# Kernel tuning notes

Measured on AMD Instinct MI355X. Metric: run time of the kernel, lower is better.

Reference implementation:

```python
import jax, jax.numpy as jnp
import numpy as np
import math

N = 12288
D = 64
SCALE0 = math.log(10.0)


def lorentz_linear(x, W, b, scale):
    # x: [N, D] -> nn.Linear then Lorentz re-normalization onto the hyperboloid
    h = x @ W.T + b
    time = jax.nn.sigmoid(h[:, :1]) * jnp.exp(scale) + 1.1  # [N, 1]
    xn = h[:, 1:]  # spatial components [N, D-1]
    sq = jnp.clip(jnp.sum(xn * xn, axis=-1, keepdims=True), 1e-8, None)
    s = (time * time - 1.0) / sq
    return jnp.concatenate([time, xn * jnp.sqrt(s)], axis=-1)


def setup_inputs() -> dict:
    key = jax.random.key(0)
    ks = jax.random.split(key, 8)
    stdv = 1.0 / math.sqrt(D)
    x = jax.random.normal(ks[0], (N, D), dtype=jnp.float32)
    # sparse-ish binary adjacency stored dense (module calls adj.to_dense())
    adj = (jax.random.uniform(ks[1], (N, N)) < 0.002).astype(jnp.float32)
    W = jax.random.uniform(ks[2], (D, D), minval=-stdv, maxval=stdv, dtype=jnp.float32)
    Wq = jax.random.uniform(ks[3], (D, D), minval=-stdv, maxval=stdv, dtype=jnp.float32)
    Wk = jax.random.uniform(ks[4], (D, D), minval=-stdv, maxval=stdv, dtype=jnp.float32)
    z = jnp.zeros((D,), dtype=jnp.float32)
    sc = jnp.asarray(SCALE0, dtype=jnp.float32)
    return {
        'x': x, 'adj': adj,
        'W': W, 'b': z, 'scale': sc,
        'Wq': Wq, 'bq': z, 'scale_q': sc,
        'Wk': Wk, 'bk': z, 'scale_k': sc,
        'att_bias': jnp.asarray(20.0, dtype=jnp.float32),
        'att_scale': jnp.asarray(math.sqrt(D), dtype=jnp.float32),
    }


def reference(x, adj, W, b, scale, Wq, bq, scale_q, Wk, bk, scale_k, att_bias, att_scale):
    # LorentzLinear
    h = lorentz_linear(x, W, b, scale)  # [N, D]
    # LorentzAgg with attention
    q = lorentz_linear(h, Wq, bq, scale_q)
    k = lorentz_linear(h, Wk, bk, scale_k)
    # cinner: Lorentzian inner product matrix (negate time component of q)
    qm = jnp.concatenate([-q[:, :1], q[:, 1:]], axis=-1)
    att = 2.0 + 2.0 * (qm @ k.T)                 # [N, N]
    att = jax.nn.sigmoid(att / att_scale + att_bias)
    att = adj * att                               # mask by adjacency
    support = att @ h                             # [N, D]
    # Lorentz self-inner: inner(v,v) = -v0^2 + sum(v_rest^2); denorm = sqrt(|-inner|)
    inner = -support[:, :1] ** 2 + jnp.sum(support[:, 1:] ** 2, axis=-1, keepdims=True)
    denorm = jnp.sqrt(jnp.clip(jnp.abs(-inner), 1e-8, None))
    return support / denorm
```

## Files before the change

### kernel.cpp

```cpp
#include <hip/hip_runtime.h>
#include <math.h>

#define N   12288
#define D   64
#define CAP 96
#define ITS ((N / 4) / 256)

typedef unsigned int uint4n __attribute__((ext_vector_type(4)));

__device__ __forceinline__ float wave_sum(float v) {
    #pragma unroll
    for (int m = 32; m >= 1; m >>= 1) v += __shfl_xor(v, m, 64);
    return v;
}
__device__ __forceinline__ float sigmoidf(float a) { return 1.0f / (1.0f + __expf(-a)); }

__global__ __launch_bounds__(256) void linear_kernel(
        const float* __restrict__ x,
        const float* __restrict__ W,  const float* __restrict__ b,  const float* __restrict__ scale,
        const float* __restrict__ Wq, const float* __restrict__ bq, const float* __restrict__ scale_q,
        const float* __restrict__ Wk, const float* __restrict__ bk, const float* __restrict__ scale_k,
        float* __restrict__ h, float* __restrict__ qm, float* __restrict__ kmat) {
    __shared__ float Wl [D * (D + 1)];
    __shared__ float Wql[D * (D + 1)];
    __shared__ float Wkl[D * (D + 1)];

    const int tid  = threadIdx.x;
    const int lane = tid & 63;
    const int w    = tid >> 6;
    const int row  = blockIdx.x * 4 + w;

    for (int idx = tid; idx < D * D; idx += 256) {
        int d = idx >> 6, kk = idx & 63;
        Wl [d * (D + 1) + kk] = W [idx];
        Wql[d * (D + 1) + kk] = Wq[idx];
        Wkl[d * (D + 1) + kk] = Wk[idx];
    }
    __syncthreads();

    float hvv;
    {
        float xv  = x[row * D + lane];
        float acc = b[lane];
        const float* wr = &Wl[lane * (D + 1)];
        #pragma unroll
        for (int kk = 0; kk < D; ++kk)
            acc = fmaf(__shfl(xv, kk, 64), wr[kk], acc);
        float h0   = __shfl(acc, 0, 64);
        float time = __expf(scale[0]) * sigmoidf(h0) + 1.1f;
        float sq   = fmaxf(wave_sum((lane == 0) ? 0.0f : acc * acc), 1e-8f);
        float r    = sqrtf((time * time - 1.0f) / sq);
        hvv = (lane == 0) ? time : acc * r;
        h[row * D + lane] = hvv;
    }

    {
        float accq = bq[lane], acck = bk[lane];
        const float* wq = &Wql[lane * (D + 1)];
        const float* wk = &Wkl[lane * (D + 1)];
        #pragma unroll
        for (int kk = 0; kk < D; ++kk) {
            float xk = __shfl(hvv, kk, 64);
            accq = fmaf(xk, wq[kk], accq);
            acck = fmaf(xk, wk[kk], acck);
        }
        {
            float h0   = __shfl(accq, 0, 64);
            float time = __expf(scale_q[0]) * sigmoidf(h0) + 1.1f;
            float sq   = fmaxf(wave_sum((lane == 0) ? 0.0f : accq * accq), 1e-8f);
            float r    = sqrtf((time * time - 1.0f) / sq);
            qm[row * D + lane] = (lane == 0) ? -time : accq * r;
        }
        {
            float h0   = __shfl(acck, 0, 64);
            float time = __expf(scale_k[0]) * sigmoidf(h0) + 1.1f;
            float sq   = fmaxf(wave_sum((lane == 0) ? 0.0f : acck * acck), 1e-8f);
            float r    = sqrtf((time * time - 1.0f) / sq);
            kmat[row * D + lane] = (lane == 0) ? time : acck * r;
        }
    }
}

__global__ __launch_bounds__(256) void adj_gather_kernel(
        const uint4n* __restrict__ adj4,
        const float* __restrict__ qm,
        const float* __restrict__ kmat,
        const float* __restrict__ h,
        const float* __restrict__ att_bias_p,
        const float* __restrict__ att_scale_p,
        float* __restrict__ out) {
    __shared__ int scols[CAP];
    __shared__ int scnt;
    __shared__ float sacc[4][D];

    int tid  = threadIdx.x;
    int row  = blockIdx.x;
    int lane = tid & 63;
    int w    = tid >> 6;
    if (tid == 0) scnt = 0;

    const uint4n* rowp = adj4 + (size_t)row * (N / 4);
    uint4n vv[ITS];
    #pragma unroll
    for (int it = 0; it < ITS; ++it)
        vv[it] = __builtin_nontemporal_load(&rowp[it * 256 + tid]);

    float qv        = qm[row * D + lane];
    float bias      = att_bias_p[0];
    float inv_scale = 1.0f / att_scale_p[0];
    __syncthreads();

    #pragma unroll
    for (int it = 0; it < ITS; ++it) {
        uint4n v = vv[it];
        if ((v.x | v.y | v.z | v.w) != 0u) {
            int t = it * 256 + tid;
            unsigned e[4] = {v.x, v.y, v.z, v.w};
            #pragma unroll
            for (int c = 0; c < 4; ++c) {
                if (e[c] != 0u) {
                    int pos = atomicAdd(&scnt, 1);
                    if (pos < CAP) scols[pos] = t * 4 + c;
                }
            }
        }
    }
    __syncthreads();

    int m = scnt; if (m > CAP) m = CAP;

    float acc = 0.0f;
    for (int n = w; n < m; n += 4) {
        int j = scols[n];
        float dot = wave_sum(qv * kmat[j * D + lane]);
        float att = sigmoidf(fmaf(2.0f + 2.0f * dot, inv_scale, bias));
        acc = fmaf(att, h[j * D + lane], acc);
    }
    sacc[w][lane] = acc;
    __syncthreads();

    if (w == 0) {
        float total = sacc[0][lane] + sacc[1][lane] + sacc[2][lane] + sacc[3][lane];
        float contrib = (lane == 0) ? -total * total : total * total;
        float inner   = wave_sum(contrib);
        float denorm  = sqrtf(fmaxf(fabsf(inner), 1e-8f));
        out[row * D + lane] = total / denorm;
    }
}

extern "C" void kernel_launch(void* const* d_in, const int* in_sizes, int n_in,
                              void* d_out, int out_size, void* d_ws, size_t ws_size,
                              hipStream_t stream) {
    const float*  x         = (const float*)d_in[0];
    const uint4n* adj       = (const uint4n*)d_in[1];
    const float*  W         = (const float*)d_in[2];
    const float*  b         = (const float*)d_in[3];
    const float*  scale     = (const float*)d_in[4];
    const float*  Wq        = (const float*)d_in[5];
    const float*  bq        = (const float*)d_in[6];
    const float*  scale_q   = (const float*)d_in[7];
    const float*  Wk        = (const float*)d_in[8];
    const float*  bk        = (const float*)d_in[9];
    const float*  scale_k   = (const float*)d_in[10];
    const float*  att_bias  = (const float*)d_in[11];
    const float*  att_scale = (const float*)d_in[12];
    float* out = (float*)d_out;

    float* h    = (float*)d_ws;
    float* qm   = h  + (size_t)N * D;
    float* kmat = qm + (size_t)N * D;

    linear_kernel<<<N / 4, 256, 0, stream>>>(x, W, b, scale,
                                             Wq, bq, scale_q, Wk, bk, scale_k,
                                             h, qm, kmat);
    adj_gather_kernel<<<N, 256, 0, stream>>>(adj, qm, kmat, h,
                                             att_bias, att_scale, out);
}
```

Baseline: 784.3 us.

## Split adjacency scan into grid-stride streaming kernel and separate gather kernel

Splits the fused per-row kernel into two. A grid-stride scan kernel streams the dense adjacency with deep unrolled nontemporal loads and appends nonzero column indices to per-row lists through global atomics. A separate gather kernel then reads those lists to compute attention and aggregate. The goal is to decouple the bandwidth-bound scan from per-row gather latency and keep more memory traffic in flight, and the gather loop also prefetches the next column index. The cost is an extra launch, global atomics and workspace for counts and columns.

```diff
diff --git a/kernel.cpp b/kernel.cpp
--- a/kernel.cpp
+++ b/kernel.cpp
@@ -4,7 +4,12 @@
 #define N   12288
 #define D   64
 #define CAP 96
-#define ITS ((N / 4) / 256)
+
+#define CHUNKS      (N * (N / 4))
+#define SCAN_BLOCKS 2048
+#define SCAN_UNROLL 8
+#define SCAN_STRIDE (SCAN_BLOCKS * 256)
+#define SCAN_PASSES (CHUNKS / (SCAN_STRIDE * SCAN_UNROLL))
 
 typedef unsigned int uint4n __attribute__((ext_vector_type(4)));
 
@@ -20,7 +25,8 @@
         const float* __restrict__ W,  const float* __restrict__ b,  const float* __restrict__ scale,
         const float* __restrict__ Wq, const float* __restrict__ bq, const float* __restrict__ scale_q,
         const float* __restrict__ Wk, const float* __restrict__ bk, const float* __restrict__ scale_k,
-        float* __restrict__ h, float* __restrict__ qm, float* __restrict__ kmat) {
+        float* __restrict__ h, float* __restrict__ qm, float* __restrict__ kmat,
+        int* __restrict__ cnt) {
     __shared__ float Wl [D * (D + 1)];
     __shared__ float Wql[D * (D + 1)];
     __shared__ float Wkl[D * (D + 1)];
@@ -29,6 +35,8 @@
     const int lane = tid & 63;
     const int w    = tid >> 6;
     const int row  = blockIdx.x * 4 + w;
+
+    if (tid < 4) cnt[blockIdx.x * 4 + tid] = 0;
 
     for (int idx = tid; idx < D * D; idx += 256) {
         int d = idx >> 6, kk = idx & 63;
@@ -81,66 +89,77 @@
     }
 }
 
-__global__ __launch_bounds__(256) void adj_gather_kernel(
+__global__ __launch_bounds__(256) void scan_kernel(
         const uint4n* __restrict__ adj4,
+        int* __restrict__ cnt,
+        int* __restrict__ cols) {
+    const int idx0 = blockIdx.x * 256 + threadIdx.x;
+    for (int p = 0; p < SCAN_PASSES; ++p) {
+        const int g0 = idx0 + p * (SCAN_STRIDE * SCAN_UNROLL);
+        uint4n v[SCAN_UNROLL];
+        #pragma unroll
+        for (int k = 0; k < SCAN_UNROLL; ++k)
+            v[k] = __builtin_nontemporal_load(&adj4[g0 + k * SCAN_STRIDE]);
+        #pragma unroll
+        for (int k = 0; k < SCAN_UNROLL; ++k) {
+            uint4n vk = v[k];
+            if ((vk.x | vk.y | vk.z | vk.w) != 0u) {
+                int g   = g0 + k * SCAN_STRIDE;
+                int row = g / (N / 4);
+                int cb  = (g - row * (N / 4)) * 4;
+                unsigned e[4] = {vk.x, vk.y, vk.z, vk.w};
+                #pragma unroll
+                for (int c = 0; c < 4; ++c) {
+                    if (e[c] != 0u) {
+                        int pos = atomicAdd(&cnt[row], 1);
+                        if (pos < CAP) cols[row * CAP + pos] = cb + c;
+                    }
+                }
+            }
+        }
+    }
+}
+
+__global__ __launch_bounds__(256) void gather_kernel(
+        const int* __restrict__ cnt,
+        const int* __restrict__ cols,
         const float* __restrict__ qm,
         const float* __restrict__ kmat,
         const float* __restrict__ h,
         const float* __restrict__ att_bias_p,
         const float* __restrict__ att_scale_p,
         float* __restrict__ out) {
-    __shared__ int scols[CAP];
-    __shared__ int scnt;
     __shared__ float sacc[4][D];
 
-    int tid  = threadIdx.x;
-    int row  = blockIdx.x;
-    int lane = tid & 63;
-    int w    = tid >> 6;
-    if (tid == 0) scnt = 0;
-
-    const uint4n* rowp = adj4 + (size_t)row * (N / 4);
-    uint4n vv[ITS];
-    #pragma unroll
-    for (int it = 0; it < ITS; ++it)
-        vv[it] = __builtin_nontemporal_load(&rowp[it * 256 + tid]);
+    const int tid  = threadIdx.x;
+    const int row  = blockIdx.x;
+    const int lane = tid & 63;
+    const int w    = tid >> 6;
 
     float qv        = qm[row * D + lane];
     float bias      = att_bias_p[0];
     float inv_scale = 1.0f / att_scale_p[0];
-    __syncthreads();
-
-    #pragma unroll
-    for (int it = 0; it < ITS; ++it) {
-        uint4n v = vv[it];
-        if ((v.x | v.y | v.z | v.w) != 0u) {
-            int t = it * 256 + tid;
-            unsigned e[4] = {v.x, v.y, v.z, v.w};
-            #pragma unroll
-            for (int c = 0; c < 4; ++c) {
-                if (e[c] != 0u) {
-                    int pos = atomicAdd(&scnt, 1);
-                    if (pos < CAP) scols[pos] = t * 4 + c;
-                }
-            }
-        }
-    }
-    __syncthreads();
-
-    int m = scnt; if (m > CAP) m = CAP;
+
+    int m = cnt[row]; if (m > CAP) m = CAP;
+    const int* cl = cols + row * CAP;
 
     float acc = 0.0f;
-    for (int n = w; n < m; n += 4) {
-        int j = scols[n];
-        float dot = wave_sum(qv * kmat[j * D + lane]);
+    int n = w;
+    int j = (n < m) ? cl[n] : 0;
+    for (; n < m; n += 4) {
+        int jn = (n + 4 < m) ? cl[n + 4] : 0;
+        float kv = kmat[j * D + lane];
+        float hv = h[j * D + lane];
+        float dot = wave_sum(qv * kv);
         float att = sigmoidf(fmaf(2.0f + 2.0f * dot, inv_scale, bias));
-        acc = fmaf(att, h[j * D + lane], acc);
+        acc = fmaf(att, hv, acc);
+        j = jn;
     }
     sacc[w][lane] = acc;
     __syncthreads();
 
     if (w == 0) {
-        float total = sacc[0][lane] + sacc[1][lane] + sacc[2][lane] + sacc[3][lane];
+        float total   = sacc[0][lane] + sacc[1][lane] + sacc[2][lane] + sacc[3][lane];
         float contrib = (lane == 0) ? -total * total : total * total;
         float inner   = wave_sum(contrib);
         float denorm  = sqrtf(fmaxf(fabsf(inner), 1e-8f));
@@ -167,12 +186,15 @@
     float* out = (float*)d_out;
 
     float* h    = (float*)d_ws;
-    float* qm   = h  + (size_t)N * D;
-    float* kmat = qm + (size_t)N * D;
+    float* qm   = h    + (size_t)N * D;
+    float* kmat = qm   + (size_t)N * D;
+    int*   cnt  = (int*)(kmat + (size_t)N * D);
+    int*   cols = cnt  + N;
 
     linear_kernel<<<N / 4, 256, 0, stream>>>(x, W, b, scale,
                                              Wq, bq, scale_q, Wk, bk, scale_k,
-                                             h, qm, kmat);
-    adj_gather_kernel<<<N, 256, 0, stream>>>(adj, qm, kmat, h,
-                                             att_bias, att_scale, out);
-}
+                                             h, qm, kmat, cnt);
+    scan_kernel<<<SCAN_BLOCKS, 256, 0, stream>>>(adj, cnt, cols);
+    gather_kernel<<<N, 256, 0, stream>>>(cnt, cols, qm, kmat, h,
+                                         att_bias, att_scale, out);
+}
```

Measured after the change: 851.9 us. 1.09x slower.
